# Kernel tuning notes

Hardware: AMD Instinct MI355X
Metric: run time of the kernel (lower is better)

Reference implementation:

```python
import jax, jax.numpy as jnp
import numpy as np

B, L, D, H = 2, 2048, 1024, 16
DK = D // H  # 64

def setup_inputs() -> dict:
    key = jax.random.key(0)
    ks = jax.random.split(key, 9)
    s = 1.0 / np.sqrt(D)
    return {
        "X":  jax.random.normal(ks[0], (B, L, D), dtype=jnp.float32),
        "WQ": jax.random.uniform(ks[1], (D, H * DK), jnp.float32, -s, s),
        "bQ": jax.random.uniform(ks[2], (H * DK,), jnp.float32, -s, s),
        "WK": jax.random.uniform(ks[3], (D, H * DK), jnp.float32, -s, s),
        "bK": jax.random.uniform(ks[4], (H * DK,), jnp.float32, -s, s),
        "WV": jax.random.uniform(ks[5], (D, H * DK), jnp.float32, -s, s),
        "bV": jax.random.uniform(ks[6], (H * DK,), jnp.float32, -s, s),
        "WO": jax.random.uniform(ks[7], (H * DK, D), jnp.float32, -s, s),
        "bO": jax.random.uniform(ks[8], (D,), jnp.float32, -s, s),
    }

def reference(X, WQ, bQ, WK, bK, WV, bV, WO, bO):
    b, l, d = X.shape
    # Linear projections, split into heads: (b, h, l, d_k)
    Q = (X @ WQ + bQ).reshape(b, l, H, DK).transpose(0, 2, 1, 3)
    K = (X @ WK + bK).reshape(b, l, H, DK).transpose(0, 2, 1, 3)
    V = (X @ WV + bV).reshape(b, l, H, DK).transpose(0, 2, 1, 3)
    # Full L x L scores (mask=None path: all-ones mask is a no-op)
    scores = jnp.einsum('bhqd,bhkd->bhqk', Q, K) / jnp.sqrt(jnp.float32(DK))
    A = jax.nn.softmax(scores, axis=-1)
    out = jnp.einsum('bhqk,bhkd->bhqd', A, V)          # (b, h, l, d_v)
    out = out.transpose(0, 2, 1, 3).reshape(b, l, H * DK)
    return out @ WO + bO
```

## Files before the change

kernel.cpp:

```cpp
#include <hip/hip_runtime.h>
#include <stdint.h>

#define BB 2
#define HH 16
#define LL 2048
#define DD 1024

typedef __bf16 b16x8 __attribute__((ext_vector_type(8)));
typedef __bf16 b16x4 __attribute__((ext_vector_type(4)));
typedef float f32x4 __attribute__((ext_vector_type(4)));

__device__ __forceinline__ short f2bf(float f) {
  unsigned u = __builtin_bit_cast(unsigned, f);
  return (short)((u + 0x7fffu + ((u >> 16) & 1u)) >> 16);
}

__device__ __forceinline__ short bfc(float f) {
  return __builtin_bit_cast(short, static_cast<__bf16>(f));
}

__device__ __forceinline__ void gl_lds16(const void* gp, void* lp) {
  __builtin_amdgcn_global_load_lds(
      (const __attribute__((address_space(1))) void*)gp,
      (__attribute__((address_space(3))) void*)lp, 16, 0, 0);
}

__global__ __launch_bounds__(256) void xcvt(const float* __restrict__ X,
                                            short* __restrict__ Xb) {
  int i = blockIdx.x * 256 + threadIdx.x;
  float4 v = ((const float4*)X)[i];
  short4 o;
  o.x = f2bf(v.x); o.y = f2bf(v.y); o.z = f2bf(v.z); o.w = f2bf(v.w);
  ((short4*)Xb)[i] = o;
}

__global__ __launch_bounds__(256) void wtrans(const float* __restrict__ W0,
                                              const float* __restrict__ W1,
                                              const float* __restrict__ W2,
                                              const float* __restrict__ W3,
                                              short* __restrict__ Wt) {
  __shared__ float t[32][33];
  const float* W = blockIdx.z == 0 ? W0 : blockIdx.z == 1 ? W1
                 : blockIdx.z == 2 ? W2 : W3;
  short* dst = Wt + (size_t)blockIdx.z * DD * DD;
  int tx = threadIdx.x & 31, ty0 = threadIdx.x >> 5;
  int nb = blockIdx.x * 32, kb = blockIdx.y * 32;
#pragma unroll
  for (int i = 0; i < 4; ++i)
    t[ty0 + i * 8][tx] = W[(size_t)(kb + ty0 + i * 8) * DD + nb + tx];
  __syncthreads();
#pragma unroll
  for (int i = 0; i < 4; ++i)
    dst[(size_t)(nb + ty0 + i * 8) * DD + kb + tx] = f2bf(t[tx][ty0 + i * 8]);
}

__global__ __launch_bounds__(256) void qkv_gemm(const short* __restrict__ Xb,
                                                const short* __restrict__ Wall,
                                                const float* __restrict__ bQ,
                                                const float* __restrict__ bK,
                                                const float* __restrict__ bV,
                                                short* __restrict__ Qo,
                                                short* __restrict__ Ko,
                                                short* __restrict__ Vto) {
  __shared__ __align__(16) short As[128 * 32];
  __shared__ __align__(16) short Bs[128 * 32];

  const int tid = threadIdx.x;
  const int lane = tid & 63;
  const int wid = tid >> 6;
  const int m0 = blockIdx.y * 128;
  const int ng = blockIdx.x * 128;
  const int sel = ng >> 10;
  const int n0 = ng & 1023;
  const short* W = Wall + (size_t)sel * DD * DD;

  const int wrow = wid >> 1, wcol = wid & 1;
  const int lrow = lane & 15;
  const int lk8 = (lane >> 4) * 8;
  const int srow = lane >> 2;
  const int scol = (lane & 3) * 8;

  f32x4 z4 = {0.f, 0.f, 0.f, 0.f};
  f32x4 acc[4][4];
#pragma unroll
  for (int i = 0; i < 4; ++i)
#pragma unroll
    for (int j = 0; j < 4; ++j) acc[i][j] = z4;

  for (int kt = 0; kt < DD; kt += 32) {
#pragma unroll
    for (int i = 0; i < 2; ++i) {
      int c = wid * 2 + i;
      gl_lds16(Xb + (size_t)(m0 + c * 16 + srow) * DD + kt + scol, As + c * 512);
      gl_lds16(W + (size_t)(n0 + c * 16 + srow) * DD + kt + scol, Bs + c * 512);
    }
    __syncthreads();
    b16x8 a[4], b[4];
#pragma unroll
    for (int i = 0; i < 4; ++i)
      a[i] = *(const b16x8*)(As + (wrow * 64 + i * 16 + lrow) * 32 + lk8);
#pragma unroll
    for (int j = 0; j < 4; ++j)
      b[j] = *(const b16x8*)(Bs + (wcol * 64 + j * 16 + lrow) * 32 + lk8);
#pragma unroll
    for (int i = 0; i < 4; ++i)
#pragma unroll
      for (int j = 0; j < 4; ++j)
        acc[i][j] = __builtin_amdgcn_mfma_f32_16x16x32_bf16(a[i], b[j], acc[i][j], 0, 0, 0);
    __syncthreads();
  }

  const float* bias = sel == 0 ? bQ : sel == 1 ? bK : bV;
  float bv[4];
#pragma unroll
  for (int j = 0; j < 4; ++j) bv[j] = bias[n0 + wcol * 64 + j * 16 + lrow];

  const int rbase = (lane >> 4) * 4;
  if (sel == 2) {
#pragma unroll
    for (int i = 0; i < 4; ++i) {
      int gm = m0 + wrow * 64 + i * 16 + rbase;
      int bb = gm >> 11, lb = gm & 2047;
      int x = lb & 63;
      int kf = x >> 4;
      int lbp = (lb & ~63) | ((kf >> 1) << 5) | (((x >> 2) & 3) << 3) | ((kf & 1) << 2);
#pragma unroll
      for (int j = 0; j < 4; ++j) {
        int gn = n0 + wcol * 64 + j * 16 + lrow;
        int h = gn >> 6, dk = gn & 63;
        short4 pk;
        pk.x = bfc(acc[i][j][0] + bv[j]);
        pk.y = bfc(acc[i][j][1] + bv[j]);
        pk.z = bfc(acc[i][j][2] + bv[j]);
        pk.w = bfc(acc[i][j][3] + bv[j]);
        *(short4*)(Vto + ((size_t)((bb * HH + h) * 64 + dk)) * LL + lbp) = pk;
      }
    }
  } else {
    short* dst = sel == 0 ? Qo : Ko;
    float sc = sel == 0 ? 0.18033688011112042f : 1.0f;
#pragma unroll
    for (int i = 0; i < 4; ++i) {
      int gm = m0 + wrow * 64 + i * 16 + rbase;
#pragma unroll
      for (int j = 0; j < 4; ++j) {
        int gn = n0 + wcol * 64 + j * 16 + lrow;
        int h = gn >> 6, dk = gn & 63;
#pragma unroll
        for (int r = 0; r < 4; ++r) {
          int m = gm + r;
          int bb = m >> 11, lq = m & 2047;
          dst[((size_t)(bb * HH + h) * LL + lq) * 64 + dk] =
              bfc((acc[i][j][r] + bv[j]) * sc);
        }
      }
    }
  }
}

__global__ __launch_bounds__(256, 2) void attn(const short* __restrict__ Qg,
                                               const short* __restrict__ Kg,
                                               const short* __restrict__ Vt,
                                               short* __restrict__ Og) {
  __shared__ __align__(16) short Ks[2][64 * 64];
  __shared__ __align__(16) short Vs[2][64 * 64];

  const int tid = threadIdx.x;
  const int lane = tid & 63;
  const int wid = tid >> 6;
  const int bh = blockIdx.y;
  const int q0 = blockIdx.x * 128 + wid * 32;

  const short* Qb = Qg + (size_t)bh * LL * 64;
  const short* Kb = Kg + (size_t)bh * LL * 64;
  const short* Vb = Vt + (size_t)bh * 64 * LL;

  const int lrow = lane & 15;
  const int hi = lane >> 4;
  const int hi8 = hi * 8;
  const int hi16b = hi * 16;
  const int r8 = lane >> 3;
  const int c8 = lane & 7;
  const int swz8 = (c8 ^ r8) * 8;

  b16x8 qf[2][2];
#pragma unroll
  for (int f = 0; f < 2; ++f)
#pragma unroll
    for (int ks = 0; ks < 2; ++ks)
      qf[f][ks] = *(const b16x8*)(Qb + (size_t)(q0 + f * 16 + lrow) * 64 + ks * 32 + hi8);

  f32x4 z4 = {0.f, 0.f, 0.f, 0.f};
  f32x4 accO[2][4];
  float m_i[2], l_i[2];
#pragma unroll
  for (int f = 0; f < 2; ++f) {
#pragma unroll
    for (int d = 0; d < 4; ++d) accO[f][d] = z4;
    m_i[f] = -1e30f; l_i[f] = 0.f;
  }

#pragma unroll
  for (int i = 0; i < 2; ++i) {
    int c = wid * 2 + i;
    gl_lds16(Kb + (size_t)(c * 8 + r8) * 64 + swz8, &Ks[0][c * 512]);
    gl_lds16(Vb + (size_t)(c * 8 + r8) * LL + swz8, &Vs[0][c * 512]);
  }
  asm volatile("s_waitcnt vmcnt(0)" ::: "memory");
  __syncthreads();

  int cur = 0;
  for (int kt = 0; kt < LL / 64; ++kt) {
    if (kt + 1 < LL / 64) {
#pragma unroll
      for (int i = 0; i < 2; ++i) {
        int c = wid * 2 + i;
        gl_lds16(Kb + (size_t)((kt + 1) * 64 + c * 8 + r8) * 64 + swz8,
                 &Ks[cur ^ 1][c * 512]);
        gl_lds16(Vb + (size_t)(c * 8 + r8) * LL + (kt + 1) * 64 + swz8,
                 &Vs[cur ^ 1][c * 512]);
      }
    }

    f32x4 sacc[2][4];
#pragma unroll
    for (int f = 0; f < 2; ++f)
#pragma unroll
      for (int kf = 0; kf < 4; ++kf) sacc[f][kf] = z4;

    __builtin_amdgcn_s_setprio(1);
#pragma unroll
    for (int kf = 0; kf < 4; ++kf) {
      int key = kf * 16 + lrow;
      int sw = (key & 7) << 4;
#pragma unroll
      for (int ks = 0; ks < 2; ++ks) {
        b16x8 kfr = *(const b16x8*)(&Ks[cur][0] + key * 64 + (((ks * 64 + hi16b) ^ sw) >> 1));
#pragma unroll
        for (int f = 0; f < 2; ++f)
          sacc[f][kf] =
              __builtin_amdgcn_mfma_f32_16x16x32_bf16(kfr, qf[f][ks], sacc[f][kf], 0, 0, 0);
      }
    }
    __builtin_amdgcn_s_setprio(0);

    float lm[2];
#pragma unroll
    for (int f = 0; f < 2; ++f) {
      float mx = sacc[f][0][0];
#pragma unroll
      for (int kf = 0; kf < 4; ++kf)
#pragma unroll
        for (int r = 0; r < 4; ++r) mx = fmaxf(mx, sacc[f][kf][r]);
      lm[f] = mx;
    }
    float w = fmaxf(lm[0] - m_i[0], lm[1] - m_i[1]);

    if (!__all(w <= 8.0f)) {
#pragma unroll
      for (int f = 0; f < 2; ++f) {
        float mx = lm[f];
        mx = fmaxf(mx, __shfl_xor(mx, 16));
        mx = fmaxf(mx, __shfl_xor(mx, 32));
        float mnew = fmaxf(m_i[f], mx);
        float corr = __builtin_amdgcn_exp2f(m_i[f] - mnew);
        l_i[f] *= corr;
        m_i[f] = mnew;
#pragma unroll
        for (int d = 0; d < 4; ++d) accO[f][d] *= corr;
      }
    }

    b16x8 pfr[2][2];
#pragma unroll
    for (int f = 0; f < 2; ++f) {
      float ps = 0.f;
#pragma unroll
      for (int kf = 0; kf < 4; ++kf)
#pragma unroll
        for (int r = 0; r < 4; ++r) {
          float p = __builtin_amdgcn_exp2f(sacc[f][kf][r] - m_i[f]);
          ps += p;
          pfr[f][kf >> 1][(kf & 1) * 4 + r] = static_cast<__bf16>(p);
        }
      l_i[f] += ps;
    }

    b16x8 vfr[4][2];
#pragma unroll
    for (int db = 0; db < 4; ++db) {
      int row = db * 16 + lrow;
      int sw = (row & 7) << 4;
#pragma unroll
      for (int ks = 0; ks < 2; ++ks)
        vfr[db][ks] = *(const b16x8*)(&Vs[cur][0] + row * 64 +
                                      (((ks * 64 + hi16b) ^ sw) >> 1));
    }

    __builtin_amdgcn_s_setprio(1);
#pragma unroll
    for (int f = 0; f < 2; ++f)
#pragma unroll
      for (int db = 0; db < 4; ++db)
#pragma unroll
        for (int ks = 0; ks < 2; ++ks)
          accO[f][db] =
              __builtin_amdgcn_mfma_f32_16x16x32_bf16(vfr[db][ks], pfr[f][ks], accO[f][db], 0, 0, 0);
    __builtin_amdgcn_s_setprio(0);

    asm volatile("s_waitcnt vmcnt(0)" ::: "memory");
    __syncthreads();
    cur ^= 1;
  }

  const int bb = bh >> 4, h = bh & 15;
#pragma unroll
  for (int f = 0; f < 2; ++f) {
    float l = l_i[f];
    l += __shfl_xor(l, 16);
    l += __shfl_xor(l, 32);
    float rl = 1.0f / l;
    int q = q0 + f * 16 + lrow;
#pragma unroll
    for (int db = 0; db < 4; ++db) {
      short4 pk;
      pk.x = bfc(accO[f][db][0] * rl);
      pk.y = bfc(accO[f][db][1] * rl);
      pk.z = bfc(accO[f][db][2] * rl);
      pk.w = bfc(accO[f][db][3] * rl);
      *(short4*)(Og + (size_t)(bb * LL + q) * DD + h * 64 + db * 16 + hi * 4) = pk;
    }
  }
}

__global__ __launch_bounds__(256) void out_gemm(const short* __restrict__ Ab,
                                                const short* __restrict__ Wt,
                                                const float* __restrict__ bO,
                                                float* __restrict__ Out) {
  __shared__ __align__(16) short As[128 * 32];
  __shared__ __align__(16) short Bs[128 * 32];

  const int tid = threadIdx.x;
  const int lane = tid & 63;
  const int wid = tid >> 6;
  const int m0 = blockIdx.y * 128;
  const int n0 = blockIdx.x * 128;

  const int wrow = wid >> 1, wcol = wid & 1;
  const int lrow = lane & 15;
  const int lk8 = (lane >> 4) * 8;
  const int srow = lane >> 2;
  const int scol = (lane & 3) * 8;

  f32x4 z4 = {0.f, 0.f, 0.f, 0.f};
  f32x4 acc[4][4];
#pragma unroll
  for (int i = 0; i < 4; ++i)
#pragma unroll
    for (int j = 0; j < 4; ++j) acc[i][j] = z4;

  for (int kt = 0; kt < DD; kt += 32) {
#pragma unroll
    for (int i = 0; i < 2; ++i) {
      int c = wid * 2 + i;
      gl_lds16(Ab + (size_t)(m0 + c * 16 + srow) * DD + kt + scol, As + c * 512);
      gl_lds16(Wt + (size_t)(n0 + c * 16 + srow) * DD + kt + scol, Bs + c * 512);
    }
    __syncthreads();
    b16x8 a[4], b[4];
#pragma unroll
    for (int i = 0; i < 4; ++i)
      a[i] = *(const b16x8*)(As + (wrow * 64 + i * 16 + lrow) * 32 + lk8);
#pragma unroll
    for (int j = 0; j < 4; ++j)
      b[j] = *(const b16x8*)(Bs + (wcol * 64 + j * 16 + lrow) * 32 + lk8);
#pragma unroll
    for (int i = 0; i < 4; ++i)
#pragma unroll
      for (int j = 0; j < 4; ++j)
        acc[i][j] = __builtin_amdgcn_mfma_f32_16x16x32_bf16(a[i], b[j], acc[i][j], 0, 0, 0);
    __syncthreads();
  }

  float bv[4];
#pragma unroll
  for (int j = 0; j < 4; ++j) bv[j] = bO[n0 + wcol * 64 + j * 16 + lrow];

  const int rbase = (lane >> 4) * 4;
#pragma unroll
  for (int i = 0; i < 4; ++i) {
    int gm = m0 + wrow * 64 + i * 16 + rbase;
#pragma unroll
    for (int j = 0; j < 4; ++j) {
      int gn = n0 + wcol * 64 + j * 16 + lrow;
#pragma unroll
      for (int r = 0; r < 4; ++r)
        Out[(size_t)(gm + r) * DD + gn] = acc[i][j][r] + bv[j];
    }
  }
}

extern "C" void kernel_launch(void* const* d_in, const int* in_sizes, int n_in,
                              void* d_out, int out_size, void* d_ws, size_t ws_size,
                              hipStream_t stream) {
  const float* X = (const float*)d_in[0];
  const float* WQ = (const float*)d_in[1];
  const float* bQ = (const float*)d_in[2];
  const float* WK = (const float*)d_in[3];
  const float* bK = (const float*)d_in[4];
  const float* WV = (const float*)d_in[5];
  const float* bV = (const float*)d_in[6];
  const float* WO = (const float*)d_in[7];
  const float* bO = (const float*)d_in[8];
  float* Out = (float*)d_out;

  if (ws_size < (size_t)24 * 1024 * 1024 * 2) return;
  short* ws = (short*)d_ws;
  short* Xb = ws;
  short* Wt = Xb + (size_t)4096 * 1024;
  short* Qb = Wt + (size_t)4 * 1024 * 1024;
  short* Kb = Qb + (size_t)4096 * 1024;
  short* Vtb = Kb + (size_t)4096 * 1024;
  short* At = Vtb + (size_t)4096 * 1024;

  hipLaunchKernelGGL(xcvt, dim3(4096), dim3(256), 0, stream, X, Xb);
  hipLaunchKernelGGL(wtrans, dim3(32, 32, 4), dim3(256), 0, stream, WQ, WK, WV, WO, Wt);
  hipLaunchKernelGGL(qkv_gemm, dim3(24, 32), dim3(256), 0, stream, Xb, Wt, bQ, bK, bV,
                     Qb, Kb, Vtb);
  hipLaunchKernelGGL(attn, dim3(16, 32), dim3(256), 0, stream, Qb, Kb, Vtb, At);
  hipLaunchKernelGGL(out_gemm, dim3(8, 32), dim3(256), 0, stream, At,
                     Wt + (size_t)3 * 1024 * 1024, bO, Out);
}
```

Before: 117.9 us.

## Triple-buffer K/V tiles in attention and remap blocks for XCD locality

Moves the attention kernel's K/V LDS staging from double to triple buffering. Tiles are prefetched two iterations ahead and the barrier waits only on the older loads (vmcnt(4)), so more global-load latency overlaps compute. It also remaps the block index so that consecutive blocks sharing one batch-head are spread in a chiplet-aware pattern, which should improve L2 reuse of K/V. In exchange it uses more LDS per block (48KB), which could reduce occupancy at 2 blocks per CU.

```diff
diff --git a/kernel.cpp b/kernel.cpp
--- a/kernel.cpp
+++ b/kernel.cpp
@@ -162,14 +162,17 @@
                                                const short* __restrict__ Kg,
                                                const short* __restrict__ Vt,
                                                short* __restrict__ Og) {
-  __shared__ __align__(16) short Ks[2][64 * 64];
-  __shared__ __align__(16) short Vs[2][64 * 64];
+  __shared__ __align__(16) short Ks[3][64 * 64];
+  __shared__ __align__(16) short Vs[3][64 * 64];
 
   const int tid = threadIdx.x;
   const int lane = tid & 63;
   const int wid = tid >> 6;
-  const int bh = blockIdx.y;
-  const int q0 = blockIdx.x * 128 + wid * 32;
+
+  const int orig = blockIdx.x + 16 * blockIdx.y;
+  const int nid = (orig & 7) * 64 + (orig >> 3);
+  const int bh = nid >> 4;
+  const int q0 = (nid & 15) * 128 + wid * 32;
 
   const short* Qb = Qg + (size_t)bh * LL * 64;
   const short* Kb = Kg + (size_t)bh * LL * 64;
@@ -200,27 +203,30 @@
     m_i[f] = -1e30f; l_i[f] = 0.f;
   }
 
-#pragma unroll
-  for (int i = 0; i < 2; ++i) {
-    int c = wid * 2 + i;
-    gl_lds16(Kb + (size_t)(c * 8 + r8) * 64 + swz8, &Ks[0][c * 512]);
-    gl_lds16(Vb + (size_t)(c * 8 + r8) * LL + swz8, &Vs[0][c * 512]);
-  }
-  asm volatile("s_waitcnt vmcnt(0)" ::: "memory");
-  __syncthreads();
+  auto stage = [&](int kt_, int buf_) {
+#pragma unroll
+    for (int i = 0; i < 2; ++i) {
+      int c = wid * 2 + i;
+      gl_lds16(Kb + (size_t)(kt_ * 64 + c * 8 + r8) * 64 + swz8, &Ks[buf_][c * 512]);
+      gl_lds16(Vb + (size_t)(c * 8 + r8) * LL + kt_ * 64 + swz8, &Vs[buf_][c * 512]);
+    }
+  };
+
+  stage(0, 0);
+  stage(1, 1);
+  asm volatile("s_waitcnt vmcnt(4)" ::: "memory");
+  __builtin_amdgcn_s_barrier();
 
   int cur = 0;
   for (int kt = 0; kt < LL / 64; ++kt) {
-    if (kt + 1 < LL / 64) {
-#pragma unroll
-      for (int i = 0; i < 2; ++i) {
-        int c = wid * 2 + i;
-        gl_lds16(Kb + (size_t)((kt + 1) * 64 + c * 8 + r8) * 64 + swz8,
-                 &Ks[cur ^ 1][c * 512]);
-        gl_lds16(Vb + (size_t)(c * 8 + r8) * LL + (kt + 1) * 64 + swz8,
-                 &Vs[cur ^ 1][c * 512]);
-      }
-    }
+    if (kt + 2 < LL / 64) {
+      int pb = cur + 2;
+      if (pb >= 3) pb -= 3;
+      stage(kt + 2, pb);
+    }
+
+    const short* ksb = &Ks[cur][0];
+    const short* vsb = &Vs[cur][0];
 
     f32x4 sacc[2][4];
 #pragma unroll
@@ -235,7 +241,7 @@
       int sw = (key & 7) << 4;
 #pragma unroll
       for (int ks = 0; ks < 2; ++ks) {
-        b16x8 kfr = *(const b16x8*)(&Ks[cur][0] + key * 64 + (((ks * 64 + hi16b) ^ sw) >> 1));
+        b16x8 kfr = *(const b16x8*)(ksb + key * 64 + (((ks * 64 + hi16b) ^ sw) >> 1));
 #pragma unroll
         for (int f = 0; f < 2; ++f)
           sacc[f][kf] =
@@ -293,8 +299,7 @@
       int sw = (row & 7) << 4;
 #pragma unroll
       for (int ks = 0; ks < 2; ++ks)
-        vfr[db][ks] = *(const b16x8*)(&Vs[cur][0] + row * 64 +
-                                      (((ks * 64 + hi16b) ^ sw) >> 1));
+        vfr[db][ks] = *(const b16x8*)(vsb + row * 64 + (((ks * 64 + hi16b) ^ sw) >> 1));
     }
 
     __builtin_amdgcn_s_setprio(1);
@@ -308,9 +313,14 @@
               __builtin_amdgcn_mfma_f32_16x16x32_bf16(vfr[db][ks], pfr[f][ks], accO[f][db], 0, 0, 0);
     __builtin_amdgcn_s_setprio(0);
 
-    asm volatile("s_waitcnt vmcnt(0)" ::: "memory");
-    __syncthreads();
-    cur ^= 1;
+    if (kt + 2 < LL / 64) {
+      asm volatile("s_waitcnt vmcnt(4)" ::: "memory");
+      __builtin_amdgcn_s_barrier();
+    } else if (kt + 1 < LL / 64) {
+      asm volatile("s_waitcnt vmcnt(0)" ::: "memory");
+      __builtin_amdgcn_s_barrier();
+    }
+    cur = cur + 1 >= 3 ? 0 : cur + 1;
   }
 
   const int bb = bh >> 4, h = bh & 15;
```

Measured after the change: 115.7 us. Within noise of the previous version (-1.9%).
